# Kernel optimization log

Hardware: AMD Instinct MI355X
Metric: run time of the kernel (lower is better)

The kernel has to match this reference:

```python
import jax, jax.numpy as jnp
import numpy as np

EPS = 1e-5


def _corner_data(x, cmin, stride, D, H, W):
    # continuous grid indices (x_idx, y_idx, z_idx); index 0 = first voxel center
    idx = (x - cmin[None, :]) / stride[None, :]
    gx, gy, gz = idx[:, 0], idx[:, 1], idx[:, 2]
    x0 = jnp.floor(gx); y0 = jnp.floor(gy); z0 = jnp.floor(gz)
    fx = jnp.clip(gx - x0, 0.0, 1.0)
    fy = jnp.clip(gy - y0, 0.0, 1.0)
    fz = jnp.clip(gz - z0, 0.0, 1.0)
    x0i = x0.astype(jnp.int32); x1i = x0i + 1
    y0i = y0.astype(jnp.int32); y1i = y0i + 1
    z0i = z0.astype(jnp.int32); z1i = z0i + 1
    # 8 trilinear corners, same order as the torch reference
    xs = jnp.stack([x0i, x1i, x0i, x1i, x0i, x1i, x0i, x1i])
    ys = jnp.stack([y0i, y0i, y1i, y1i, y0i, y0i, y1i, y1i])
    zs = jnp.stack([z0i, z0i, z0i, z0i, z1i, z1i, z1i, z1i])
    wx = jnp.stack([1 - fx, fx, 1 - fx, fx, 1 - fx, fx, 1 - fx, fx])
    wy = jnp.stack([1 - fy, 1 - fy, fy, fy, 1 - fy, 1 - fy, fy, fy])
    wz = jnp.stack([1 - fz, 1 - fz, 1 - fz, 1 - fz, fz, fz, fz, fz])
    ws = wx * wy * wz                                    # (8, N)
    valid = (xs >= 0) & (xs < W) & (ys >= 0) & (ys < H) & (zs >= 0) & (zs < D)
    xi = jnp.clip(xs, 0, W - 1)
    yi = jnp.clip(ys, 0, H - 1)
    zi = jnp.clip(zs, 0, D - 1)
    flat = zi * (H * W) + yi * W + xi                    # (8, N) flat voxel index
    return flat, ws * valid.astype(ws.dtype)


def setup_inputs() -> dict:
    key = jax.random.key(0)
    ks = jax.random.split(key, 20)
    N = 200000; B = 4; D = H = W = 64; CG = 64; NC = 128; HID = 128
    h = jax.random.normal(ks[0], (N, NC), jnp.float32)
    x = jax.random.uniform(ks[1], (N, 3), jnp.float32) * 63.0
    grid = jax.random.normal(ks[2], (B, CG, D, H, W), jnp.float32)
    node_batch = jax.random.randint(ks[3], (N,), 0, B, jnp.int32)
    coordinates_min = jnp.zeros((3,), jnp.float32)
    spatial_stride = jnp.ones((3,), jnp.float32)
    s = 0.05
    params = dict(
        w1=jax.random.normal(ks[4], (HID, NC + CG), jnp.float32) * s,
        b1=jax.random.normal(ks[5], (HID,), jnp.float32) * s,
        w2=jax.random.normal(ks[6], (NC, HID), jnp.float32) * s,
        b2=jax.random.normal(ks[7], (NC,), jnp.float32) * s,
        ln_g=1.0 + jax.random.normal(ks[8], (NC,), jnp.float32) * s,
        ln_b=jax.random.normal(ks[9], (NC,), jnp.float32) * s,
        wn2g=jax.random.normal(ks[10], (CG, NC), jnp.float32) * s,
        bn2g=jax.random.normal(ks[11], (CG,), jnp.float32) * s,
        wc1=jax.random.normal(ks[12], (CG, 2 * CG), jnp.float32) * s,
        bc1=jax.random.normal(ks[13], (CG,), jnp.float32) * s,
        wc2=jax.random.normal(ks[14], (CG, CG), jnp.float32) * s,
        bc2=jax.random.normal(ks[15], (CG,), jnp.float32) * s,
        in_g=1.0 + jax.random.normal(ks[16], (CG,), jnp.float32) * s,
        in_b=jax.random.normal(ks[17], (CG,), jnp.float32) * s,
    )
    return dict(h=h, x=x, grid=grid, node_batch=node_batch,
                coordinates_min=coordinates_min, spatial_stride=spatial_stride, **params)


def reference(h, x, grid, node_batch, coordinates_min, spatial_stride,
              w1, b1, w2, b2, ln_g, ln_b, wn2g, bn2g, wc1, bc1, wc2, bc2, in_g, in_b):
    B, Cg, D, H, W = grid.shape
    DHW = D * H * W
    flat, w = _corner_data(x, coordinates_min, spatial_stride, D, H, W)  # (8,N)

    # grid -> node: trilinear gather (== grid_sample, align_corners=True, zeros padding)
    gflat = grid.reshape(B, Cg, DHW).transpose(0, 2, 1)                  # (B,DHW,Cg)
    vals = gflat[node_batch[None, :], flat]                              # (8,N,Cg)
    sampled = jnp.einsum('kn,knc->nc', w, vals)                          # (N,Cg)

    # node MLP + residual + LayerNorm
    z = jnp.concatenate([h, sampled], axis=-1)
    m = jax.nn.silu(z @ w1.T + b1) @ w2.T + b2
    hn = h + m
    mu = hn.mean(-1, keepdims=True)
    var = hn.var(-1, keepdims=True)
    hn = (hn - mu) / jnp.sqrt(var + EPS) * ln_g + ln_b

    # node -> grid: trilinear scatter-add splat of projected features
    proj = hn @ wn2g.T + bn2g                                            # (N,Cg)
    gidx = node_batch[None, :] * DHW + flat                              # (8,N) global flat index
    contrib = w[:, :, None] * proj[None]                                 # (8,N,Cg)
    vol = jnp.zeros((B * DHW, Cg), grid.dtype).at[gidx.reshape(-1)].add(contrib.reshape(-1, Cg))
    splat = vol.reshape(B, D, H, W, Cg).transpose(0, 4, 1, 2, 3)         # (B,Cg,D,H,W)

    # grid MLP (1x1x1 convs) + residual + InstanceNorm (affine)
    cat = jnp.concatenate([grid, splat], axis=1)                         # (B,2Cg,D,H,W)
    g1 = jax.nn.silu(jnp.einsum('bcdhw,oc->bodhw', cat, wc1) + bc1[None, :, None, None, None])
    g2 = jnp.einsum('bcdhw,oc->bodhw', g1, wc2) + bc2[None, :, None, None, None]
    gr = grid + g2
    mu = gr.mean((2, 3, 4), keepdims=True)
    var = gr.var((2, 3, 4), keepdims=True)
    gr = (gr - mu) / jnp.sqrt(var + EPS) * in_g[None, :, None, None, None] + in_b[None, :, None, None, None]
    return hn, gr
```

## Files before the change

kernel.cpp:

```cpp
#include <hip/hip_runtime.h>
#include <hip/hip_fp16.h>
#include <cstdint>

#define NNODES 200000
#define NCH 128
#define NBATCH 4
#define DHW 262144
#define K1 192

#define VOLH_OFF  0ull
#define VOLH_BYTES 134217728ull
#define PART_OFF  134217728ull
#define STAT_OFF  142606336ull
#define NWF_OFF   142608384ull
#define WF_OFF    142706688ull
#define PRJ_OFF   142731264ull
#define CFG_OFF   168331264ull
#define CWG_OFF   174731264ull
#define GT_OFF    257931264ull
#define GRH_OFF   392149056ull

typedef _Float16 h2 __attribute__((ext_vector_type(2)));
typedef __fp16  fp16x2 __attribute__((ext_vector_type(2)));
typedef _Float16 f16x8 __attribute__((ext_vector_type(8)));
typedef float f32x4 __attribute__((ext_vector_type(4)));

__device__ __forceinline__ uint32_t pack_h2(float a, float b){
  fp16x2 p = __builtin_amdgcn_cvt_pkrtz(a, b);
  return __builtin_bit_cast(uint32_t, p);
}
__device__ __forceinline__ h2 as_h2(uint32_t w){ return __builtin_bit_cast(h2, w); }
__device__ __forceinline__ float siluf(float a){ return a / (1.f + __expf(-a)); }
__device__ __forceinline__ f32x4 mfma16(uint4 a, uint4 b, f32x4 c){
  return __builtin_amdgcn_mfma_f32_16x16x32_f16(
      __builtin_bit_cast(f16x8, a), __builtin_bit_cast(f16x8, b), c, 0, 0, 0);
}
__device__ __forceinline__ void atomic_pk_add_f16(uint32_t* addr, uint32_t val){
  asm volatile("global_atomic_pk_add_f16 %0, %1, off"
               :: "v"(addr), "v"(val) : "memory");
}

__global__ void fill_kernel(uint4* __restrict__ p, size_t n4)
{
  size_t stride = (size_t)gridDim.x * 256;
  const uint4 z = make_uint4(0u, 0u, 0u, 0u);
  for (size_t i = blockIdx.x * 256 + threadIdx.x; i < n4; i += stride) p[i] = z;
}

__global__ void pack_nw(const float* __restrict__ w1, const float* __restrict__ w2,
                        const float* __restrict__ wn2g, uint32_t* __restrict__ nwf)
{
  int t = blockIdx.x * 256 + threadIdx.x;
  int q = t & 3, lane = (t >> 2) & 63;
  int vl = lane & 15, g = lane >> 4;
  if (t < 12288) {
    int f = t >> 8, s = f % 6, tt = f / 6;
    int o = tt * 16 + vl, k = s * 32 + g * 8 + 2 * q;
    nwf[t] = pack_h2(w1[o * K1 + k], w1[o * K1 + k + 1]);
  } else if (t < 20480) {
    int f = (t - 12288) >> 8, s = f & 3, tt = f >> 2;
    int o = tt * 16 + vl, k = s * 32 + g * 8 + 2 * q;
    nwf[t] = pack_h2(w2[o * 128 + k], w2[o * 128 + k + 1]);
  } else if (t < 24576) {
    int f = (t - 20480) >> 8, s = f & 3, tt = f >> 2;
    int o = tt * 16 + vl, k = s * 32 + g * 8 + 2 * q;
    nwf[t] = pack_h2(wn2g[o * 128 + k], wn2g[o * 128 + k + 1]);
  }
}

__global__ void pack_wc(const float* __restrict__ wc1, const float* __restrict__ wc2,
                        uint32_t* __restrict__ wf)
{
  int t = blockIdx.x * 256 + threadIdx.x;
  if (t < 4096) {
    int q = t & 3, lane = (t >> 2) & 63, f = t >> 8;
    int s = f & 3, tt = f >> 2;
    int o = tt * 16 + (lane & 15);
    int k = s * 32 + (lane >> 4) * 8 + 2 * q;
    wf[t] = pack_h2(wc1[o * 128 + k], wc1[o * 128 + k + 1]);
  } else if (t < 6144) {
    int u = t - 4096;
    int q = u & 3, lane = (u >> 2) & 63, f = u >> 8;
    int s = f & 1, tt = f >> 1;
    int o = tt * 16 + (lane & 15);
    int k = s * 32 + (lane >> 4) * 8 + 2 * q;
    wf[t] = pack_h2(wc2[o * 64 + k], wc2[o * 64 + k + 1]);
  }
}

__global__ void transpose_kernel(const float* __restrict__ grid, uint32_t* __restrict__ gt)
{
  __shared__ float tile[64][65];
  int bx = blockIdx.x;
  int b = bx >> 12;
  int dhw0 = (bx & 4095) << 6;
  const float* gbase = grid + ((size_t)b * 64) * DHW + dhw0;
  int c0 = threadIdx.x >> 6, d = threadIdx.x & 63;
  #pragma unroll
  for (int i = 0; i < 16; ++i)
    tile[i * 4 + c0][d] = gbase[(size_t)(i * 4 + c0) * DHW + d];
  __syncthreads();
  uint32_t* tb = gt + ((size_t)b * DHW + dhw0) * 32;
  int p = threadIdx.x & 31, r0 = threadIdx.x >> 5;
  #pragma unroll
  for (int i = 0; i < 8; ++i) {
    int dd = i * 8 + r0;
    tb[(size_t)dd * 32 + p] = pack_h2(tile[2 * p][dd], tile[2 * p + 1][dd]);
  }
}

__launch_bounds__(256, 2)
__global__ void node_fused(const float* __restrict__ h, const float* __restrict__ x,
                           const uint32_t* __restrict__ gridT, const int* __restrict__ nbat,
                           const float* __restrict__ cmin, const float* __restrict__ sstr,
                           const uint32_t* __restrict__ nwf,
                           const float* __restrict__ b1, const float* __restrict__ b2,
                           const float* __restrict__ ln_g, const float* __restrict__ ln_b,
                           const float* __restrict__ bn2g,
                           float* __restrict__ hn_out, uint32_t* __restrict__ prjv,
                           int* __restrict__ cfg, float* __restrict__ cwg)
{
  __shared__ __align__(16) uint32_t zt[64][100];
  __shared__ __align__(16) uint32_t g1z[64][68];
  __shared__ float wpart[4][64][2];
  __shared__ float cwS[64][8];
  __shared__ int   cfS[64][8];

  const int tid = threadIdx.x;
  const int lane = tid & 63, w = tid >> 6;
  const int g = lane >> 4, vl = lane & 15;
  const int n0 = blockIdx.x * 64;

  {
    const float c0 = cmin[0], c1 = cmin[1], c2 = cmin[2];
    const float st0 = sstr[0], st1 = sstr[1], st2 = sstr[2];
    int nd = tid & 63, j = tid >> 6;
    int n = n0 + nd;
    float gx = (x[n * 3 + 0] - c0) / st0;
    float gy = (x[n * 3 + 1] - c1) / st1;
    float gz = (x[n * 3 + 2] - c2) / st2;
    float fx0 = floorf(gx), fy0 = floorf(gy), fz0 = floorf(gz);
    float fx = fminf(fmaxf(gx - fx0, 0.f), 1.f);
    float fy = fminf(fmaxf(gy - fy0, 0.f), 1.f);
    float fz = fminf(fmaxf(gz - fz0, 0.f), 1.f);
    int ix0 = (int)fx0, iy0 = (int)fy0, iz0 = (int)fz0;
    int b = nbat[n];
    int cf2[2]; float cw2[2];
    #pragma unroll
    for (int kk = 0; kk < 2; ++kk) {
      int k = 2 * j + kk;
      int xi = (k & 1) ? ix0 + 1 : ix0;
      int yi = (k & 2) ? iy0 + 1 : iy0;
      int zi = (k & 4) ? iz0 + 1 : iz0;
      float wx = (k & 1) ? fx : 1.f - fx;
      float wy = (k & 2) ? fy : 1.f - fy;
      float wz = (k & 4) ? fz : 1.f - fz;
      bool valid = (xi >= 0) & (xi < 64) & (yi >= 0) & (yi < 64) & (zi >= 0) & (zi < 64);
      int xc = min(max(xi, 0), 63), yc = min(max(yi, 0), 63), zc = min(max(zi, 0), 63);
      cw2[kk] = valid ? wx * wy * wz : 0.f;
      cf2[kk] = b * DHW + ((zc << 12) | (yc << 6) | xc);
      cwS[nd][k] = cw2[kk];
      cfS[nd][k] = cf2[kk];
    }
    *(int2*)&cfg[(size_t)n * 8 + 2 * j] = make_int2(cf2[0], cf2[1]);
    *(float2*)&cwg[(size_t)n * 8 + 2 * j] = make_float2(cw2[0], cw2[1]);
  }
  {
    int nd = tid >> 2, q = tid & 3;
    const float4* hp = (const float4*)&h[(size_t)(n0 + nd) * NCH + q * 32];
    #pragma unroll
    for (int r = 0; r < 8; ++r) {
      float4 f = hp[r];
      zt[nd][q * 16 + 2 * r]     = pack_h2(f.x, f.y);
      zt[nd][q * 16 + 2 * r + 1] = pack_h2(f.z, f.w);
    }
  }
  __syncthreads();

  {
    const int p = lane & 31, kb = lane >> 5;
    #pragma unroll 4
    for (int i = 0; i < 16; ++i) {
      int nd = w * 16 + i;
      float slo = 0.f, shi = 0.f;
      #pragma unroll
      for (int jj = 0; jj < 4; ++jj) {
        int k = 2 * jj + kb;
        int   cfk = cfS[nd][k];
        float cwk = cwS[nd][k];
        h2 gv = as_h2(gridT[(size_t)cfk * 32 + p]);
        slo = fmaf(cwk, (float)gv.x, slo);
        shi = fmaf(cwk, (float)gv.y, shi);
      }
      slo += __shfl_xor(slo, 32);
      shi += __shfl_xor(shi, 32);
      if (lane < 32) zt[nd][64 + p] = pack_h2(slo, shi);
    }
  }
  __syncthreads();

  const uint4* nf4 = (const uint4*)nwf;
  uint4 a1f[2][6], a2f[2][4], apf[4];
  #pragma unroll
  for (int j = 0; j < 2; ++j) {
    int tt = 2 * w + j;
    #pragma unroll
    for (int s = 0; s < 6; ++s) a1f[j][s] = nf4[(tt * 6 + s) * 64 + lane];
    #pragma unroll
    for (int s = 0; s < 4; ++s) a2f[j][s] = nf4[3072 + (tt * 4 + s) * 64 + lane];
  }
  #pragma unroll
  for (int s = 0; s < 4; ++s) apf[s] = nf4[5120 + (w * 4 + s) * 64 + lane];

  float4 b1r[2], b2r[2], lgr[2], lbr[2], bnr;
  #pragma unroll
  for (int j = 0; j < 2; ++j) {
    int c = (2 * w + j) * 16 + g * 4;
    b1r[j] = *(const float4*)&b1[c];
    b2r[j] = *(const float4*)&b2[c];
    lgr[j] = *(const float4*)&ln_g[c];
    lbr[j] = *(const float4*)&ln_b[c];
  }
  bnr = *(const float4*)&bn2g[w * 16 + g * 4];

  #pragma unroll
  for (int nc = 0; nc < 4; ++nc) {
    uint4 bfr[6];
    #pragma unroll
    for (int s = 0; s < 6; ++s) bfr[s] = *(const uint4*)&zt[nc * 16 + vl][s * 16 + g * 4];
    f32x4 acc[2];
    acc[0][0]=b1r[0].x; acc[0][1]=b1r[0].y; acc[0][2]=b1r[0].z; acc[0][3]=b1r[0].w;
    acc[1][0]=b1r[1].x; acc[1][1]=b1r[1].y; acc[1][2]=b1r[1].z; acc[1][3]=b1r[1].w;
    #pragma unroll
    for (int s = 0; s < 6; ++s) {
      acc[0] = mfma16(a1f[0][s], bfr[s], acc[0]);
      acc[1] = mfma16(a1f[1][s], bfr[s], acc[1]);
    }
    #pragma unroll
    for (int j = 0; j < 2; ++j) {
      uint2 pr;
      pr.x = pack_h2(siluf(acc[j][0]), siluf(acc[j][1]));
      pr.y = pack_h2(siluf(acc[j][2]), siluf(acc[j][3]));
      *(uint2*)&g1z[nc * 16 + vl][(2 * w + j) * 8 + g * 2] = pr;
    }
  }
  __syncthreads();

  float hnv[2][4][4];
  #pragma unroll
  for (int nc = 0; nc < 4; ++nc) {
    uint4 bfr[4];
    #pragma unroll
    for (int s = 0; s < 4; ++s) bfr[s] = *(const uint4*)&g1z[nc * 16 + vl][s * 16 + g * 4];
    f32x4 acc[2];
    acc[0][0]=b2r[0].x; acc[0][1]=b2r[0].y; acc[0][2]=b2r[0].z; acc[0][3]=b2r[0].w;
    acc[1][0]=b2r[1].x; acc[1][1]=b2r[1].y; acc[1][2]=b2r[1].z; acc[1][3]=b2r[1].w;
    #pragma unroll
    for (int s = 0; s < 4; ++s) {
      acc[0] = mfma16(a2f[0][s], bfr[s], acc[0]);
      acc[1] = mfma16(a2f[1][s], bfr[s], acc[1]);
    }
    float s_ = 0.f, q_ = 0.f;
    #pragma unroll
    for (int j = 0; j < 2; ++j) {
      uint2 hp = *(const uint2*)&zt[nc * 16 + vl][(2 * w + j) * 8 + g * 2];
      h2 p0 = as_h2(hp.x), p1 = as_h2(hp.y);
      float v0 = acc[j][0] + (float)p0.x;
      float v1 = acc[j][1] + (float)p0.y;
      float v2 = acc[j][2] + (float)p1.x;
      float v3 = acc[j][3] + (float)p1.y;
      hnv[j][nc][0] = v0; hnv[j][nc][1] = v1; hnv[j][nc][2] = v2; hnv[j][nc][3] = v3;
      s_ += v0 + v1 + v2 + v3;
      q_ += v0 * v0 + v1 * v1 + v2 * v2 + v3 * v3;
    }
    s_ += __shfl_xor(s_, 16); q_ += __shfl_xor(q_, 16);
    s_ += __shfl_xor(s_, 32); q_ += __shfl_xor(q_, 32);
    if (lane < 16) { wpart[w][nc * 16 + lane][0] = s_; wpart[w][nc * 16 + lane][1] = q_; }
  }
  __syncthreads();

  #pragma unroll
  for (int nc = 0; nc < 4; ++nc) {
    int node = nc * 16 + vl;
    float2 p0 = *(const float2*)&wpart[0][node][0];
    float2 p1 = *(const float2*)&wpart[1][node][0];
    float2 p2 = *(const float2*)&wpart[2][node][0];
    float2 p3 = *(const float2*)&wpart[3][node][0];
    float mu = (p0.x + p1.x + p2.x + p3.x) * (1.f / 128.f);
    float var = (p0.y + p1.y + p2.y + p3.y) * (1.f / 128.f) - mu * mu;
    float rstd = rsqrtf(var + 1e-5f);
    #pragma unroll
    for (int j = 0; j < 2; ++j) {
      float y0 = (hnv[j][nc][0] - mu) * rstd * ((const float*)&lgr[j])[0] + ((const float*)&lbr[j])[0];
      float y1 = (hnv[j][nc][1] - mu) * rstd * ((const float*)&lgr[j])[1] + ((const float*)&lbr[j])[1];
      float y2 = (hnv[j][nc][2] - mu) * rstd * ((const float*)&lgr[j])[2] + ((const float*)&lbr[j])[2];
      float y3 = (hnv[j][nc][3] - mu) * rstd * ((const float*)&lgr[j])[3] + ((const float*)&lbr[j])[3];
      *(float4*)&hn_out[(size_t)(n0 + node) * NCH + (2 * w + j) * 16 + g * 4] =
          make_float4(y0, y1, y2, y3);
      uint2 pz;
      pz.x = pack_h2(y0, y1);
      pz.y = pack_h2(y2, y3);
      *(uint2*)&g1z[node][(2 * w + j) * 8 + g * 2] = pz;
    }
  }
  __syncthreads();

  #pragma unroll
  for (int nc = 0; nc < 4; ++nc) {
    int node = nc * 16 + vl;
    uint4 bfr[4];
    #pragma unroll
    for (int s = 0; s < 4; ++s) bfr[s] = *(const uint4*)&g1z[node][s * 16 + g * 4];
    f32x4 acc;
    acc[0]=bnr.x; acc[1]=bnr.y; acc[2]=bnr.z; acc[3]=bnr.w;
    #pragma unroll
    for (int s = 0; s < 4; ++s) acc = mfma16(apf[s], bfr[s], acc);
    uint2 pr;
    pr.x = pack_h2(acc[0], acc[1]);
    pr.y = pack_h2(acc[2], acc[3]);
    *(uint2*)&prjv[(size_t)(n0 + node) * 32 + w * 8 + g * 2] = pr;
  }
}

__launch_bounds__(256)
__global__ void scatter_kernel(const int* __restrict__ cfg, const float* __restrict__ cwg,
                               const uint32_t* __restrict__ prjv, uint32_t* __restrict__ volh)
{
  const int lane = threadIdx.x & 63;
  const int half = lane >> 5, c = lane & 31;
  const int wid = (blockIdx.x * 256 + threadIdx.x) >> 6;
  const int nw = (gridDim.x * 256) >> 6;
  const int total = NNODES * 8 / 2;
  for (int it = wid; it < total; it += nw) {
    int pr = it * 2 + half;
    int node = pr >> 3, k = pr & 7;
    float wv = cwg[node * 8 + k];
    if (wv != 0.f) {
      int gidx = cfg[node * 8 + k];
      h2 p = as_h2(prjv[(size_t)node * 32 + c]);
      uint32_t v = pack_h2(wv * (float)p.x, wv * (float)p.y);
      atomic_pk_add_f16(&volh[(size_t)gidx * 32 + c], v);
    }
  }
}

__launch_bounds__(256, 2)
__global__ void voxel_kernel(const uint32_t* __restrict__ gridT, const uint32_t* __restrict__ volh,
                             const uint32_t* __restrict__ wf, const float* __restrict__ bc1,
                             const float* __restrict__ bc2,
                             _Float16* __restrict__ grh, float* __restrict__ partials)
{
  __shared__ __align__(16) uint32_t xt[64][68];
  __shared__ __align__(16) uint32_t g1b[4][16][36];
  __shared__ float part_s[4][128];

  const int tid = threadIdx.x;
  const int lane = tid & 63, wv = tid >> 6;
  const int g = lane >> 4, vl = lane & 15;
  const int b = blockIdx.x >> 12;
  const int dhw0 = (blockIdx.x & 4095) << 6;

  {
    const uint32_t* gt = gridT + ((size_t)b * DHW + dhw0) * 32;
    #pragma unroll
    for (int it = 0; it < 2; ++it) {
      int u = it * 256 + tid;
      int v = u >> 3, p4 = u & 7;
      *(uint4*)&xt[v][4 * p4] = *(const uint4*)&gt[(size_t)v * 32 + 4 * p4];
    }
  }
  {
    const uint32_t* vb = volh + ((size_t)b * DHW + dhw0) * 32;
    #pragma unroll
    for (int it = 0; it < 2; ++it) {
      int u = it * 256 + tid;
      int v = u >> 3, p4 = u & 7;
      *(uint4*)&xt[v][32 + 4 * p4] = *(const uint4*)&vb[(size_t)v * 32 + 4 * p4];
    }
  }

  const uint4* wf4 = (const uint4*)wf;
  uint4 w1f[4][4], w2f[4][2];
  #pragma unroll
  for (int t = 0; t < 4; ++t)
    #pragma unroll
    for (int s = 0; s < 4; ++s)
      w1f[t][s] = wf4[(t * 4 + s) * 64 + lane];
  #pragma unroll
  for (int t = 0; t < 4; ++t)
    #pragma unroll
    for (int s = 0; s < 2; ++s)
      w2f[t][s] = wf4[1024 + (t * 2 + s) * 64 + lane];

  f32x4 acc1[4];
  #pragma unroll
  for (int t = 0; t < 4; ++t) {
    #pragma unroll
    for (int r = 0; r < 4; ++r) acc1[t][r] = bc1[t * 16 + g * 4 + r];
  }

  __syncthreads();

  const int v = wv * 16 + vl;
  #pragma unroll
  for (int s = 0; s < 4; ++s) {
    uint4 xb = *(const uint4*)&xt[v][s * 16 + g * 4];
    #pragma unroll
    for (int t = 0; t < 4; ++t) acc1[t] = mfma16(w1f[t][s], xb, acc1[t]);
  }

  #pragma unroll
  for (int t = 0; t < 4; ++t) {
    uint2 pr;
    pr.x = pack_h2(siluf(acc1[t][0]), siluf(acc1[t][1]));
    pr.y = pack_h2(siluf(acc1[t][2]), siluf(acc1[t][3]));
    *(uint2*)&g1b[wv][vl][t * 8 + g * 2] = pr;
  }
  asm volatile("s_waitcnt lgkmcnt(0)" ::: "memory");

  f32x4 acc2[4];
  #pragma unroll
  for (int t = 0; t < 4; ++t) {
    #pragma unroll
    for (int r = 0; r < 4; ++r) acc2[t][r] = bc2[t * 16 + g * 4 + r];
  }
  #pragma unroll
  for (int s = 0; s < 2; ++s) {
    uint4 gv = *(const uint4*)&g1b[wv][vl][s * 16 + g * 4];
    #pragma unroll
    for (int t = 0; t < 4; ++t) acc2[t] = mfma16(w2f[t][s], gv, acc2[t]);
  }

  const int dhw = dhw0 + v;
  #pragma unroll
  for (int t = 0; t < 4; ++t) {
    uint2 gp = *(const uint2*)&xt[v][t * 8 + g * 2];
    h2 g0 = as_h2(gp.x), g1 = as_h2(gp.y);
    float gc[4] = {(float)g0.x, (float)g0.y, (float)g1.x, (float)g1.y};
    #pragma unroll
    for (int r = 0; r < 4; ++r) {
      int o = t * 16 + g * 4 + r;
      float grv = gc[r] + acc2[t][r];
      grh[(size_t)(b * 64 + o) * DHW + dhw] = (_Float16)grv;
      float sv = grv, qv = grv * grv;
      sv += __shfl_xor(sv, 1, 64); qv += __shfl_xor(qv, 1, 64);
      sv += __shfl_xor(sv, 2, 64); qv += __shfl_xor(qv, 2, 64);
      sv += __shfl_xor(sv, 4, 64); qv += __shfl_xor(qv, 4, 64);
      sv += __shfl_xor(sv, 8, 64); qv += __shfl_xor(qv, 8, 64);
      if (vl == 0) { part_s[wv][2 * o] = sv; part_s[wv][2 * o + 1] = qv; }
    }
  }
  __syncthreads();
  if (tid < 128)
    partials[(size_t)blockIdx.x * 128 + tid] =
        part_s[0][tid] + part_s[1][tid] + part_s[2][tid] + part_s[3][tid];
}

__global__ void stats_kernel(const float* __restrict__ partials, const float* __restrict__ in_g,
                             const float* __restrict__ in_b, float* __restrict__ stats)
{
  int bo = blockIdx.x;
  int b = bo >> 6, o = bo & 63;
  float s = 0.f, q = 0.f;
  for (int k = threadIdx.x; k < 4096; k += 256) {
    const float* pp = partials + (size_t)(b * 4096 + k) * 128 + 2 * o;
    s += pp[0]; q += pp[1];
  }
  __shared__ float sred[256], qred[256];
  sred[threadIdx.x] = s; qred[threadIdx.x] = q;
  __syncthreads();
  for (int st = 128; st >= 1; st >>= 1) {
    if (threadIdx.x < st) { sred[threadIdx.x] += sred[threadIdx.x + st]; qred[threadIdx.x] += qred[threadIdx.x + st]; }
    __syncthreads();
  }
  if (threadIdx.x == 0) {
    float mu = sred[0] * (1.f / (float)DHW);
    float var = qred[0] * (1.f / (float)DHW) - mu * mu;
    float rstd = rsqrtf(var + 1e-5f);
    float scale = rstd * in_g[o];
    stats[2 * bo] = scale;
    stats[2 * bo + 1] = in_b[o] - mu * scale;
  }
}

__global__ void norm_kernel(const uint32_t* __restrict__ grh, const float* __restrict__ stats,
                            float* __restrict__ gr)
{
  const size_t total = (size_t)NBATCH * 64 * DHW / 2;
  size_t stride = (size_t)gridDim.x * 256;
  for (size_t i = blockIdx.x * 256 + threadIdx.x; i < total; i += stride) {
    int bo = (int)(i >> 17);
    float scale = stats[2 * bo], shift = stats[2 * bo + 1];
    h2 p = as_h2(grh[i]);
    float2 o;
    o.x = fmaf((float)p.x, scale, shift);
    o.y = fmaf((float)p.y, scale, shift);
    *(float2*)&gr[2 * i] = o;
  }
}

extern "C" void kernel_launch(void* const* d_in, const int* in_sizes, int n_in,
                              void* d_out, int out_size, void* d_ws, size_t ws_size,
                              hipStream_t stream)
{
  const float* h     = (const float*)d_in[0];
  const float* x     = (const float*)d_in[1];
  const float* grid  = (const float*)d_in[2];
  const int*   nbat  = (const int*)d_in[3];
  const float* cmin  = (const float*)d_in[4];
  const float* sstr  = (const float*)d_in[5];
  const float* w1    = (const float*)d_in[6];
  const float* b1    = (const float*)d_in[7];
  const float* w2    = (const float*)d_in[8];
  const float* b2    = (const float*)d_in[9];
  const float* ln_g  = (const float*)d_in[10];
  const float* ln_b  = (const float*)d_in[11];
  const float* wn2g  = (const float*)d_in[12];
  const float* bn2g  = (const float*)d_in[13];
  const float* wc1   = (const float*)d_in[14];
  const float* bc1   = (const float*)d_in[15];
  const float* wc2   = (const float*)d_in[16];
  const float* bc2   = (const float*)d_in[17];
  const float* in_g  = (const float*)d_in[18];
  const float* in_b  = (const float*)d_in[19];

  float* hn_out = (float*)d_out;
  float* gr_out = (float*)d_out + (size_t)NNODES * NCH;

  char* ws = (char*)d_ws;
  uint32_t* volh     = (uint32_t*)(ws + VOLH_OFF);
  float*    partials = (float*)(ws + PART_OFF);
  float*    stats    = (float*)(ws + STAT_OFF);
  uint32_t* nwf      = (uint32_t*)(ws + NWF_OFF);
  uint32_t* wf       = (uint32_t*)(ws + WF_OFF);
  uint32_t* prjv     = (uint32_t*)(ws + PRJ_OFF);
  int*      cfg      = (int*)(ws + CFG_OFF);
  float*    cwg      = (float*)(ws + CWG_OFF);
  uint32_t* gridT    = (uint32_t*)(ws + GT_OFF);
  _Float16* grh      = (_Float16*)(ws + GRH_OFF);

  fill_kernel<<<2048, 256, 0, stream>>>((uint4*)volh, VOLH_BYTES / 16);
  pack_nw<<<96, 256, 0, stream>>>(w1, w2, wn2g, nwf);
  pack_wc<<<24, 256, 0, stream>>>(wc1, wc2, wf);
  transpose_kernel<<<16384, 256, 0, stream>>>(grid, gridT);
  node_fused<<<3125, 256, 0, stream>>>(h, x, gridT, nbat, cmin, sstr, nwf,
                                       b1, b2, ln_g, ln_b, bn2g, hn_out, prjv, cfg, cwg);
  scatter_kernel<<<2048, 256, 0, stream>>>(cfg, cwg, prjv, volh);
  voxel_kernel<<<16384, 256, 0, stream>>>(gridT, volh, wf, bc1, bc2, grh, partials);
  stats_kernel<<<256, 256, 0, stream>>>(partials, in_g, in_b, stats);
  norm_kernel<<<8192, 256, 0, stream>>>((const uint32_t*)grh, stats, gr_out);
}
```

Baseline: 676.6 us.

## Fuse scatter-add splat into node kernel, merge weight packing, widen norm

Moves the trilinear atomic scatter into node_fused: projected features are kept in shared memory and each wave issues the fp16 packed atomics directly, which removes the prjv/cfg/cwg global round trip and one kernel launch. The two weight-packing kernels are merged into a single launch, and norm_kernel now reads 4 halves and writes a float4 per thread. In exchange, node_fused carries the atomic traffic, which may lengthen its runtime and reduce overlap, and the atomics now happen in node order within each block.

```diff
diff --git a/kernel.cpp b/kernel.cpp
--- a/kernel.cpp
+++ b/kernel.cpp
@@ -14,9 +14,6 @@
 #define STAT_OFF  142606336ull
 #define NWF_OFF   142608384ull
 #define WF_OFF    142706688ull
-#define PRJ_OFF   142731264ull
-#define CFG_OFF   168331264ull
-#define CWG_OFF   174731264ull
 #define GT_OFF    257931264ull
 #define GRH_OFF   392149056ull
 
@@ -47,44 +44,44 @@
   for (size_t i = blockIdx.x * 256 + threadIdx.x; i < n4; i += stride) p[i] = z;
 }
 
-__global__ void pack_nw(const float* __restrict__ w1, const float* __restrict__ w2,
-                        const float* __restrict__ wn2g, uint32_t* __restrict__ nwf)
+__global__ void pack_all(const float* __restrict__ w1, const float* __restrict__ w2,
+                         const float* __restrict__ wn2g,
+                         const float* __restrict__ wc1, const float* __restrict__ wc2,
+                         uint32_t* __restrict__ nwf, uint32_t* __restrict__ wf)
 {
   int t = blockIdx.x * 256 + threadIdx.x;
-  int q = t & 3, lane = (t >> 2) & 63;
-  int vl = lane & 15, g = lane >> 4;
-  if (t < 12288) {
-    int f = t >> 8, s = f % 6, tt = f / 6;
-    int o = tt * 16 + vl, k = s * 32 + g * 8 + 2 * q;
-    nwf[t] = pack_h2(w1[o * K1 + k], w1[o * K1 + k + 1]);
-  } else if (t < 20480) {
-    int f = (t - 12288) >> 8, s = f & 3, tt = f >> 2;
-    int o = tt * 16 + vl, k = s * 32 + g * 8 + 2 * q;
-    nwf[t] = pack_h2(w2[o * 128 + k], w2[o * 128 + k + 1]);
-  } else if (t < 24576) {
-    int f = (t - 20480) >> 8, s = f & 3, tt = f >> 2;
-    int o = tt * 16 + vl, k = s * 32 + g * 8 + 2 * q;
-    nwf[t] = pack_h2(wn2g[o * 128 + k], wn2g[o * 128 + k + 1]);
-  }
-}
-
-__global__ void pack_wc(const float* __restrict__ wc1, const float* __restrict__ wc2,
-                        uint32_t* __restrict__ wf)
-{
-  int t = blockIdx.x * 256 + threadIdx.x;
-  if (t < 4096) {
-    int q = t & 3, lane = (t >> 2) & 63, f = t >> 8;
-    int s = f & 3, tt = f >> 2;
-    int o = tt * 16 + (lane & 15);
-    int k = s * 32 + (lane >> 4) * 8 + 2 * q;
-    wf[t] = pack_h2(wc1[o * 128 + k], wc1[o * 128 + k + 1]);
-  } else if (t < 6144) {
-    int u = t - 4096;
-    int q = u & 3, lane = (u >> 2) & 63, f = u >> 8;
-    int s = f & 1, tt = f >> 1;
-    int o = tt * 16 + (lane & 15);
-    int k = s * 32 + (lane >> 4) * 8 + 2 * q;
-    wf[t] = pack_h2(wc2[o * 64 + k], wc2[o * 64 + k + 1]);
+  if (t < 24576) {
+    int q = t & 3, lane = (t >> 2) & 63;
+    int vl = lane & 15, g = lane >> 4;
+    if (t < 12288) {
+      int f = t >> 8, s = f % 6, tt = f / 6;
+      int o = tt * 16 + vl, k = s * 32 + g * 8 + 2 * q;
+      nwf[t] = pack_h2(w1[o * K1 + k], w1[o * K1 + k + 1]);
+    } else if (t < 20480) {
+      int f = (t - 12288) >> 8, s = f & 3, tt = f >> 2;
+      int o = tt * 16 + vl, k = s * 32 + g * 8 + 2 * q;
+      nwf[t] = pack_h2(w2[o * 128 + k], w2[o * 128 + k + 1]);
+    } else {
+      int f = (t - 20480) >> 8, s = f & 3, tt = f >> 2;
+      int o = tt * 16 + vl, k = s * 32 + g * 8 + 2 * q;
+      nwf[t] = pack_h2(wn2g[o * 128 + k], wn2g[o * 128 + k + 1]);
+    }
+  } else if (t < 30720) {
+    int u = t - 24576;
+    if (u < 4096) {
+      int q = u & 3, lane = (u >> 2) & 63, f = u >> 8;
+      int s = f & 3, tt = f >> 2;
+      int o = tt * 16 + (lane & 15);
+      int k = s * 32 + (lane >> 4) * 8 + 2 * q;
+      wf[u] = pack_h2(wc1[o * 128 + k], wc1[o * 128 + k + 1]);
+    } else {
+      int uu = u - 4096;
+      int q = uu & 3, lane = (uu >> 2) & 63, f = uu >> 8;
+      int s = f & 1, tt = f >> 1;
+      int o = tt * 16 + (lane & 15);
+      int k = s * 32 + (lane >> 4) * 8 + 2 * q;
+      wf[u] = pack_h2(wc2[o * 64 + k], wc2[o * 64 + k + 1]);
+    }
   }
 }
 
@@ -117,8 +114,7 @@
                            const float* __restrict__ b1, const float* __restrict__ b2,
                            const float* __restrict__ ln_g, const float* __restrict__ ln_b,
                            const float* __restrict__ bn2g,
-                           float* __restrict__ hn_out, uint32_t* __restrict__ prjv,
-                           int* __restrict__ cfg, float* __restrict__ cwg)
+                           float* __restrict__ hn_out, uint32_t* __restrict__ volh)
 {
   __shared__ __align__(16) uint32_t zt[64][100];
   __shared__ __align__(16) uint32_t g1z[64][68];
@@ -145,7 +141,6 @@
     float fz = fminf(fmaxf(gz - fz0, 0.f), 1.f);
     int ix0 = (int)fx0, iy0 = (int)fy0, iz0 = (int)fz0;
     int b = nbat[n];
-    int cf2[2]; float cw2[2];
     #pragma unroll
     for (int kk = 0; kk < 2; ++kk) {
       int k = 2 * j + kk;
@@ -157,13 +152,9 @@
       float wz = (k & 4) ? fz : 1.f - fz;
       bool valid = (xi >= 0) & (xi < 64) & (yi >= 0) & (yi < 64) & (zi >= 0) & (zi < 64);
       int xc = min(max(xi, 0), 63), yc = min(max(yi, 0), 63), zc = min(max(zi, 0), 63);
-      cw2[kk] = valid ? wx * wy * wz : 0.f;
-      cf2[kk] = b * DHW + ((zc << 12) | (yc << 6) | xc);
-      cwS[nd][k] = cw2[kk];
-      cfS[nd][k] = cf2[kk];
-    }
-    *(int2*)&cfg[(size_t)n * 8 + 2 * j] = make_int2(cf2[0], cf2[1]);
-    *(float2*)&cwg[(size_t)n * 8 + 2 * j] = make_float2(cw2[0], cw2[1]);
+      cwS[nd][k] = valid ? wx * wy * wz : 0.f;
+      cfS[nd][k] = b * DHW + ((zc << 12) | (yc << 6) | xc);
+    }
   }
   {
     int nd = tid >> 2, q = tid & 3;
@@ -318,28 +309,26 @@
     uint2 pr;
     pr.x = pack_h2(acc[0], acc[1]);
     pr.y = pack_h2(acc[2], acc[3]);
-    *(uint2*)&prjv[(size_t)(n0 + node) * 32 + w * 8 + g * 2] = pr;
-  }
-}
-
-__launch_bounds__(256)
-__global__ void scatter_kernel(const int* __restrict__ cfg, const float* __restrict__ cwg,
-                               const uint32_t* __restrict__ prjv, uint32_t* __restrict__ volh)
-{
-  const int lane = threadIdx.x & 63;
-  const int half = lane >> 5, c = lane & 31;
-  const int wid = (blockIdx.x * 256 + threadIdx.x) >> 6;
-  const int nw = (gridDim.x * 256) >> 6;
-  const int total = NNODES * 8 / 2;
-  for (int it = wid; it < total; it += nw) {
-    int pr = it * 2 + half;
-    int node = pr >> 3, k = pr & 7;
-    float wv = cwg[node * 8 + k];
-    if (wv != 0.f) {
-      int gidx = cfg[node * 8 + k];
-      h2 p = as_h2(prjv[(size_t)node * 32 + c]);
-      uint32_t v = pack_h2(wv * (float)p.x, wv * (float)p.y);
-      atomic_pk_add_f16(&volh[(size_t)gidx * 32 + c], v);
+    *(uint2*)&zt[node][w * 8 + g * 2] = pr;
+  }
+  __syncthreads();
+
+  {
+    const int half = lane >> 5, c = lane & 31;
+    for (int i = 0; i < 16; ++i) {
+      int node = w * 16 + i;
+      uint32_t pz = zt[node][c];
+      h2 p = as_h2(pz);
+      #pragma unroll
+      for (int kk = 0; kk < 4; ++kk) {
+        int k = 2 * kk + half;
+        float wv = cwS[node][k];
+        if (wv != 0.f) {
+          int gidx = cfS[node][k];
+          uint32_t v = pack_h2(wv * (float)p.x, wv * (float)p.y);
+          atomic_pk_add_f16(&volh[(size_t)gidx * 32 + c], v);
+        }
+      }
     }
   }
 }
@@ -483,19 +472,22 @@
   }
 }
 
-__global__ void norm_kernel(const uint32_t* __restrict__ grh, const float* __restrict__ stats,
+__global__ void norm_kernel(const uint2* __restrict__ grh2, const float* __restrict__ stats,
                             float* __restrict__ gr)
 {
-  const size_t total = (size_t)NBATCH * 64 * DHW / 2;
+  const size_t total = (size_t)NBATCH * 64 * DHW / 4;
   size_t stride = (size_t)gridDim.x * 256;
   for (size_t i = blockIdx.x * 256 + threadIdx.x; i < total; i += stride) {
-    int bo = (int)(i >> 17);
+    int bo = (int)(i >> 16);
     float scale = stats[2 * bo], shift = stats[2 * bo + 1];
-    h2 p = as_h2(grh[i]);
-    float2 o;
-    o.x = fmaf((float)p.x, scale, shift);
-    o.y = fmaf((float)p.y, scale, shift);
-    *(float2*)&gr[2 * i] = o;
+    uint2 u = grh2[i];
+    h2 p0 = as_h2(u.x), p1 = as_h2(u.y);
+    float4 o;
+    o.x = fmaf((float)p0.x, scale, shift);
+    o.y = fmaf((float)p0.y, scale, shift);
+    o.z = fmaf((float)p1.x, scale, shift);
+    o.w = fmaf((float)p1.y, scale, shift);
+    *(float4*)&gr[4 * i] = o;
   }
 }
 
@@ -533,20 +525,15 @@
   float*    stats    = (float*)(ws + STAT_OFF);
   uint32_t* nwf      = (uint32_t*)(ws + NWF_OFF);
   uint32_t* wf       = (uint32_t*)(ws + WF_OFF);
-  uint32_t* prjv     = (uint32_t*)(ws + PRJ_OFF);
-  int*      cfg      = (int*)(ws + CFG_OFF);
-  float*    cwg      = (float*)(ws + CWG_OFF);
   uint32_t* gridT    = (uint32_t*)(ws + GT_OFF);
   _Float16* grh      = (_Float16*)(ws + GRH_OFF);
 
   fill_kernel<<<2048, 256, 0, stream>>>((uint4*)volh, VOLH_BYTES / 16);
-  pack_nw<<<96, 256, 0, stream>>>(w1, w2, wn2g, nwf);
-  pack_wc<<<24, 256, 0, stream>>>(wc1, wc2, wf);
+  pack_all<<<120, 256, 0, stream>>>(w1, w2, wn2g, wc1, wc2, nwf, wf);
   transpose_kernel<<<16384, 256, 0, stream>>>(grid, gridT);
   node_fused<<<3125, 256, 0, stream>>>(h, x, gridT, nbat, cmin, sstr, nwf,
-                                       b1, b2, ln_g, ln_b, bn2g, hn_out, prjv, cfg, cwg);
-  scatter_kernel<<<2048, 256, 0, stream>>>(cfg, cwg, prjv, volh);
+                                       b1, b2, ln_g, ln_b, bn2g, hn_out, volh);
   voxel_kernel<<<16384, 256, 0, stream>>>(gridT, volh, wf, bc1, bc2, grh, partials);
   stats_kernel<<<256, 256, 0, stream>>>(partials, in_g, in_b, stats);
-  norm_kernel<<<8192, 256, 0, stream>>>((const uint32_t*)grh, stats, gr_out);
-}
+  norm_kernel<<<8192, 256, 0, stream>>>((const uint2*)grh, stats, gr_out);
+}
```

After: 603.3 us. -10.8%, faster.
